# Kernel optimization log

Measured on AMD Instinct MI355X. Metric: run time of the kernel, lower is better.

Reference implementation:

```python
import jax, jax.numpy as jnp
import numpy as np

N = 100000      # nodes
E = 1600000     # edges (avg degree 16)
D_IN = 128
H = 256
OUT = 20
EPS = 1e-5      # BatchNorm1d default eps


def setup_inputs() -> dict:
    key = jax.random.key(0)
    ks = jax.random.split(key, 16)
    s = 0.05  # keep activations bounded across stacked layers
    x = jax.random.normal(ks[0], (N, D_IN), jnp.float32)
    edge_index = jax.random.randint(ks[1], (2, E), 0, N, dtype=jnp.int32)
    W0 = jax.random.normal(ks[2], (D_IN, H), jnp.float32) * s
    W1 = jax.random.normal(ks[3], (H, H), jnp.float32) * s
    W2 = jax.random.normal(ks[4], (H, H), jnp.float32) * s
    W3 = jax.random.normal(ks[5], (H, OUT), jnp.float32) * s
    b0 = jnp.zeros((H,), jnp.float32)
    b1 = jnp.zeros((H,), jnp.float32)
    b2 = jnp.zeros((H,), jnp.float32)
    b3 = jnp.zeros((OUT,), jnp.float32)
    gamma = jnp.ones((3, H), jnp.float32) + 0.1 * jax.random.normal(ks[6], (3, H), jnp.float32)
    beta = 0.1 * jax.random.normal(ks[7], (3, H), jnp.float32)
    run_mean = 0.05 * jax.random.normal(ks[8], (3, H), jnp.float32)
    run_var = jnp.ones((3, H), jnp.float32) + 0.5 * jax.random.uniform(ks[9], (3, H), jnp.float32)
    return {"x": x, "edge_index": edge_index,
            "W0": W0, "b0": b0, "W1": W1, "b1": b1, "W2": W2, "b2": b2,
            "W3": W3, "b3": b3, "gamma": gamma, "beta": beta,
            "run_mean": run_mean, "run_var": run_var}


def _gcn_aggregate(h, src, dst, dinv_sqrt):
    # PyG GCNConv: add self-loops, sym-normalized scatter-add of projected feats.
    coef = (dinv_sqrt[src] * dinv_sqrt[dst])[:, None]          # [E,1]
    agg = jax.ops.segment_sum(h[src] * coef, dst, num_segments=N)
    # self-loop contribution: norm = deg^-1 for i==j
    return agg + h * (dinv_sqrt * dinv_sqrt)[:, None]


def reference(x, edge_index, W0, b0, W1, b1, W2, b2, W3, b3,
              gamma, beta, run_mean, run_var):
    src, dst = edge_index[0], edge_index[1]
    # degree with self-loops (counted on dst, as PyG does on col index)
    deg = jax.ops.segment_sum(jnp.ones((E,), jnp.float32), dst, num_segments=N) + 1.0
    dinv_sqrt = jax.lax.rsqrt(deg)

    h = x
    for i, (W, b) in enumerate([(W0, b0), (W1, b1), (W2, b2)]):
        h = _gcn_aggregate(h @ W, src, dst, dinv_sqrt) + b
        # BatchNorm1d in eval mode (running stats), then ReLU; dropout is identity in eval
        h = (h - run_mean[i]) * jax.lax.rsqrt(run_var[i] + EPS) * gamma[i] + beta[i]
        h = jax.nn.relu(h)
    h = _gcn_aggregate(h @ W3, src, dst, dinv_sqrt) + b3
    return h
```

## Files before the change

kernel.cpp:

```cpp
#include <hip/hip_runtime.h>
#include <hip/hip_bf16.h>
#include <stdint.h>

#define NN 100000
#define NE 1600000
#define BNEPS 1e-5f
#define NBKT 391
#define NBA  256
#define CHUNK ((NE + NBA - 1) / NBA)

using short8 = __attribute__((ext_vector_type(8))) short;
using f32x4  = __attribute__((ext_vector_type(4))) float;

__device__ __forceinline__ float b2f(ushort u) {
  union { uint32_t u; float f; } c; c.u = ((uint32_t)u) << 16; return c.f;
}
__device__ __forceinline__ ushort f2bf(float f) {
  union { float f; uint32_t u; } c; c.f = f;
  uint32_t r = (c.u + 0x7FFFu + ((c.u >> 16) & 1u)) >> 16;
  return (ushort)r;
}
__device__ __forceinline__ uint pk(float a, float b) {
  return (uint)f2bf(a) | ((uint)f2bf(b) << 16);
}
__device__ __forceinline__ void gload16(const void* g, void* lds) {
  __builtin_amdgcn_global_load_lds((const __attribute__((address_space(1))) void*)g,
                                   (__attribute__((address_space(3))) void*)lds,
                                   16, 0, 0);
}
__device__ __forceinline__ void add16(float* a, uint4 q) {
  a[0] += b2f((ushort)(q.x & 0xFFFF)); a[1] += b2f((ushort)(q.x >> 16));
  a[2] += b2f((ushort)(q.y & 0xFFFF)); a[3] += b2f((ushort)(q.y >> 16));
  a[4] += b2f((ushort)(q.z & 0xFFFF)); a[5] += b2f((ushort)(q.z >> 16));
  a[6] += b2f((ushort)(q.w & 0xFFFF)); a[7] += b2f((ushort)(q.w >> 16));
}
__device__ __forceinline__ void set16(float* a, uint4 q) {
  a[0] = b2f((ushort)(q.x & 0xFFFF)); a[1] = b2f((ushort)(q.x >> 16));
  a[2] = b2f((ushort)(q.y & 0xFFFF)); a[3] = b2f((ushort)(q.y >> 16));
  a[4] = b2f((ushort)(q.z & 0xFFFF)); a[5] = b2f((ushort)(q.z >> 16));
  a[6] = b2f((ushort)(q.w & 0xFFFF)); a[7] = b2f((ushort)(q.w >> 16));
}

__global__ __launch_bounds__(256) void k_hist(const int* __restrict__ dst, int* __restrict__ ghist) {
  __shared__ int h[NBKT];
  for (int t = threadIdx.x; t < NBKT; t += 256) h[t] = 0;
  __syncthreads();
  int e0 = blockIdx.x * CHUNK;
  int e1 = e0 + CHUNK; if (e1 > NE) e1 = NE;
  for (int e = e0 + threadIdx.x; e < e1; e += 256)
    atomicAdd(&h[((uint)dst[e]) >> 8], 1);
  __syncthreads();
  for (int t = threadIdx.x; t < NBKT; t += 256) ghist[t * NBA + blockIdx.x] = h[t];
}

__global__ __launch_bounds__(256) void k_gscanA(const int* __restrict__ ghist, int* __restrict__ gbase,
                                                int* __restrict__ btot) {
  __shared__ int s[256];
  int t = threadIdx.x, b = blockIdx.x;
  int d = ghist[b * NBA + t];
  s[t] = d; __syncthreads();
  int val = d;
  for (int sh = 1; sh < 256; sh <<= 1) {
    int tv = (t >= sh) ? s[t - sh] : 0;
    __syncthreads();
    val += tv; s[t] = val;
    __syncthreads();
  }
  gbase[b * NBA + t] = val - d;
  if (t == 255) btot[b] = val;
}

__global__ __launch_bounds__(512) void k_bscan(const int* __restrict__ btot, int* __restrict__ bbase,
                                               int* __restrict__ offs) {
  __shared__ int s[512];
  int t = threadIdx.x;
  int d = (t < NBKT) ? btot[t] : 0;
  s[t] = d; __syncthreads();
  int val = d;
  for (int sh = 1; sh < 512; sh <<= 1) {
    int tv = (t >= sh) ? s[t - sh] : 0;
    __syncthreads();
    val += tv; s[t] = val;
    __syncthreads();
  }
  if (t < NBKT) bbase[t] = val - d;
  if (t == 0) offs[NN] = NE;
}

__global__ __launch_bounds__(256) void k_scatter(const int* __restrict__ src, const int* __restrict__ dst,
                                                 const int* __restrict__ bbase, const int* __restrict__ gbase,
                                                 uint* __restrict__ bpack) {
  __shared__ int lbase[NBKT];
  for (int t = threadIdx.x; t < NBKT; t += 256)
    lbase[t] = bbase[t] + gbase[t * NBA + blockIdx.x];
  __syncthreads();
  int e0 = blockIdx.x * CHUNK;
  int e1 = e0 + CHUNK; if (e1 > NE) e1 = NE;
  for (int e = e0 + threadIdx.x; e < e1; e += 256) {
    int d = dst[e];
    int pos = atomicAdd(&lbase[((uint)d) >> 8], 1);
    bpack[pos] = ((uint)(d & 255) << 17) | (uint)src[e];
  }
}

__global__ __launch_bounds__(256) void k_bucketB(const uint* __restrict__ bpack, const int* __restrict__ btot,
                                                 const int* __restrict__ bbase, int* __restrict__ csrc,
                                                 int* __restrict__ offs, float* __restrict__ dinv) {
  __shared__ int hist[256];
  __shared__ int sc[256];
  __shared__ int loc[256];
  int b = blockIdx.x, t = threadIdx.x;
  int cnt = btot[b], base = bbase[b];
  const uint* bp = bpack + base;
  hist[t] = 0; __syncthreads();
  for (int i = t; i < cnt; i += 256) atomicAdd(&hist[bp[i] >> 17], 1);
  __syncthreads();
  int d = hist[t];
  sc[t] = d; __syncthreads();
  int val = d;
  for (int sh = 1; sh < 256; sh <<= 1) {
    int tv = (t >= sh) ? sc[t - sh] : 0;
    __syncthreads();
    val += tv; sc[t] = val;
    __syncthreads();
  }
  loc[t] = val - d;
  int n = b * 256 + t;
  if (n < NN) {
    offs[n] = base + val - d;
    dinv[n] = rsqrtf((float)d + 1.0f);
  }
  __syncthreads();
  for (int i = t; i < cnt; i += 256) {
    uint p = bp[i];
    int l = p >> 17, s = p & 0x1FFFF;
    int pos = atomicAdd(&loc[l], 1);
    csrc[base + pos] = s;
  }
}

__global__ __launch_bounds__(256) void k_prep(
    const float* __restrict__ W0, const float* __restrict__ W1, const float* __restrict__ W2,
    const float* __restrict__ W3, const float* __restrict__ b0, const float* __restrict__ b1,
    const float* __restrict__ b2, const float* __restrict__ gamma, const float* __restrict__ beta,
    const float* __restrict__ rm, const float* __restrict__ rv,
    ushort* __restrict__ W0t, ushort* __restrict__ W1t, ushort* __restrict__ W2t,
    ushort* __restrict__ W3t, float* __restrict__ bnA, float* __restrict__ bnB) {
  int tid = blockIdx.x * blockDim.x + threadIdx.x;
  int nthr = gridDim.x * blockDim.x;
  for (int i = tid; i < 256 * 128; i += nthr) { int m = i >> 7, k = i & 127; W0t[i] = f2bf(W0[k * 256 + m]); }
  for (int i = tid; i < 256 * 256; i += nthr) {
    int m = i >> 8, k = i & 255;
    W1t[i] = f2bf(W1[k * 256 + m]);
    W2t[i] = f2bf(W2[k * 256 + m]);
  }
  for (int i = tid; i < 32 * 256; i += nthr) {
    int m = i >> 8, k = i & 255;
    W3t[i] = (m < 20) ? f2bf(W3[k * 20 + m]) : (ushort)0;
  }
  for (int i = tid; i < 3 * 256; i += nthr) {
    int l = i >> 8, c = i & 255;
    float A = gamma[i] * rsqrtf(rv[i] + BNEPS);
    float bb = (l == 0) ? b0[c] : (l == 1) ? b1[c] : b2[c];
    bnA[i] = A;
    bnB[i] = (bb - rm[i]) * A + beta[i];
  }
}

__global__ __launch_bounds__(256) void k_convx(const float4* __restrict__ x, uint2* __restrict__ xb,
                                               const float* __restrict__ dinv) {
  int stride = gridDim.x * blockDim.x;
  const int n4 = NN * 128 / 4;
  for (int i = blockIdx.x * blockDim.x + threadIdx.x; i < n4; i += stride) {
    float4 f = x[i];
    float dv = dinv[i >> 5];
    uint2 o;
    o.x = pk(f.x * dv, f.y * dv);
    o.y = pk(f.z * dv, f.w * dv);
    xb[i] = o;
  }
}


__global__ __launch_bounds__(256) void k_agg256(const ushort* __restrict__ Z,
                                                const int* __restrict__ offs, const int* __restrict__ csrc,
                                                const float* __restrict__ dinv, ushort* __restrict__ Outb) {
  int wave = threadIdx.x >> 6, lane = threadIdx.x & 63;
  int v = blockIdx.x * 4 + wave;
  if (v >= NN) return;
  float dv = dinv[v];
  int p = lane >> 5, fl = lane & 31;
  const uint4* Z4 = reinterpret_cast<const uint4*>(Z);
  float acc[8];
  if (p == 0) {
    set16(acc, Z4[(size_t)v * 32 + fl]);
  } else {
#pragma unroll
    for (int j = 0; j < 8; ++j) acc[j] = 0.0f;
  }
  int e1 = offs[v + 1];
  int e = offs[v] + p;
  for (; e + 6 < e1; e += 8) {
    int u0 = csrc[e], u1 = csrc[e + 2], u2 = csrc[e + 4], u3 = csrc[e + 6];
    uint4 q0 = Z4[(size_t)u0 * 32 + fl];
    uint4 q1 = Z4[(size_t)u1 * 32 + fl];
    uint4 q2 = Z4[(size_t)u2 * 32 + fl];
    uint4 q3 = Z4[(size_t)u3 * 32 + fl];
    add16(acc, q0); add16(acc, q1); add16(acc, q2); add16(acc, q3);
  }
  for (; e < e1; e += 2) add16(acc, Z4[(size_t)csrc[e] * 32 + fl]);
#pragma unroll
  for (int j = 0; j < 8; ++j) acc[j] += __shfl_xor(acc[j], 32);
  int o = p * 4;
  uint2 w;
  w.x = pk(acc[o + 0] * dv, acc[o + 1] * dv);
  w.y = pk(acc[o + 2] * dv, acc[o + 3] * dv);
  reinterpret_cast<uint2*>(Outb)[(size_t)v * 64 + fl * 2 + p] = w;
}

__global__ __launch_bounds__(256) void k_agg128(const ushort* __restrict__ Z,
                                                const int* __restrict__ offs, const int* __restrict__ csrc,
                                                const float* __restrict__ dinv, ushort* __restrict__ Outb) {
  int wave = threadIdx.x >> 6, lane = threadIdx.x & 63;
  int v = blockIdx.x * 4 + wave;
  if (v >= NN) return;
  float dv = dinv[v];
  int q = lane >> 4, fl = lane & 15;
  const uint4* Z4 = reinterpret_cast<const uint4*>(Z);
  float acc[8];
  if (q == 0) {
    set16(acc, Z4[(size_t)v * 16 + fl]);
  } else {
#pragma unroll
    for (int j = 0; j < 8; ++j) acc[j] = 0.0f;
  }
  int e1 = offs[v + 1];
  int e = offs[v] + q;
  for (; e + 12 < e1; e += 16) {
    int u0 = csrc[e], u1 = csrc[e + 4], u2 = csrc[e + 8], u3 = csrc[e + 12];
    uint4 q0 = Z4[(size_t)u0 * 16 + fl];
    uint4 q1 = Z4[(size_t)u1 * 16 + fl];
    uint4 q2 = Z4[(size_t)u2 * 16 + fl];
    uint4 q3 = Z4[(size_t)u3 * 16 + fl];
    add16(acc, q0); add16(acc, q1); add16(acc, q2); add16(acc, q3);
  }
  for (; e < e1; e += 4) add16(acc, Z4[(size_t)csrc[e] * 16 + fl]);
#pragma unroll
  for (int j = 0; j < 8; ++j) {
    acc[j] += __shfl_xor(acc[j], 16);
    acc[j] += __shfl_xor(acc[j], 32);
  }
  uint w = pk(acc[2 * q] * dv, acc[2 * q + 1] * dv);
  reinterpret_cast<uint*>(Outb)[(size_t)v * 64 + fl * 4 + q] = w;
}

__global__ __launch_bounds__(256) void k_aggfin(const ushort* __restrict__ Z,
                                                const int* __restrict__ offs, const int* __restrict__ csrc,
                                                const float* __restrict__ dinv, const float* __restrict__ b3,
                                                float* __restrict__ out) {
  int wave = threadIdx.x >> 6, lane = threadIdx.x & 63;
  int v = blockIdx.x * 4 + wave;
  if (v >= NN) return;
  float dv = dinv[v];
  int s = lane >> 3, fl = lane & 7;
  const uint2* Z2 = reinterpret_cast<const uint2*>(Z);
  float acc[4];
  if (s == 0) {
    uint2 qq = Z2[(size_t)v * 8 + fl];
    acc[0] = b2f((ushort)(qq.x & 0xFFFF)); acc[1] = b2f((ushort)(qq.x >> 16));
    acc[2] = b2f((ushort)(qq.y & 0xFFFF)); acc[3] = b2f((ushort)(qq.y >> 16));
  } else {
    acc[0] = acc[1] = acc[2] = acc[3] = 0.0f;
  }
  int e1 = offs[v + 1];
  int e = offs[v] + s;
  for (; e + 8 < e1; e += 16) {
    int u0 = csrc[e], u1 = csrc[e + 8];
    uint2 q0 = Z2[(size_t)u0 * 8 + fl];
    uint2 q1 = Z2[(size_t)u1 * 8 + fl];
    acc[0] += b2f((ushort)(q0.x & 0xFFFF)) + b2f((ushort)(q1.x & 0xFFFF));
    acc[1] += b2f((ushort)(q0.x >> 16))    + b2f((ushort)(q1.x >> 16));
    acc[2] += b2f((ushort)(q0.y & 0xFFFF)) + b2f((ushort)(q1.y & 0xFFFF));
    acc[3] += b2f((ushort)(q0.y >> 16))    + b2f((ushort)(q1.y >> 16));
  }
  for (; e < e1; e += 8) {
    uint2 qq = Z2[(size_t)csrc[e] * 8 + fl];
    acc[0] += b2f((ushort)(qq.x & 0xFFFF)); acc[1] += b2f((ushort)(qq.x >> 16));
    acc[2] += b2f((ushort)(qq.y & 0xFFFF)); acc[3] += b2f((ushort)(qq.y >> 16));
  }
#pragma unroll
  for (int j = 0; j < 4; ++j) {
    acc[j] += __shfl_xor(acc[j], 8);
    acc[j] += __shfl_xor(acc[j], 16);
    acc[j] += __shfl_xor(acc[j], 32);
  }
  if (s == 0 && fl < 5) {
    float4 w;
    w.x = acc[0] * dv + b3[fl * 4 + 0];
    w.y = acc[1] * dv + b3[fl * 4 + 1];
    w.z = acc[2] * dv + b3[fl * 4 + 2];
    w.w = acc[3] * dv + b3[fl * 4 + 3];
    *reinterpret_cast<float4*>(out + (size_t)v * 20 + fl * 4) = w;
  }
}

template<int KT, bool EPI, bool SCALE>
__global__ __launch_bounds__(256) void k_gemm2(const ushort* __restrict__ A,
                                               const ushort* __restrict__ Bt,
                                               ushort* __restrict__ Out,
                                               const float* __restrict__ bnA,
                                               const float* __restrict__ bnB,
                                               const float* __restrict__ dinv) {
  constexpr int BK = 64;
  constexpr int NT = KT / BK;
  __shared__ ushort Ald[2][128 * 64];
  __shared__ ushort Bld[2][128 * 64];
  int tid = threadIdx.x;
  int lane = tid & 63;
  int wave = tid >> 6;
  int wm = wave >> 1, wn = wave & 1;
  size_t row0 = (size_t)blockIdx.y * 128;
  int col0 = blockIdx.x * 128;
  int laneLo = lane & 15, laneHi = lane >> 4;

  f32x4 acc[4][4];
#pragma unroll
  for (int i = 0; i < 4; ++i)
#pragma unroll
    for (int j = 0; j < 4; ++j)
#pragma unroll
      for (int r = 0; r < 4; ++r) acc[i][j][r] = 0.0f;

  auto stage = [&](int buf, int k0) {
#pragma unroll
    for (int is = 0; is < 4; ++is) {
      int idx = is * 256 + tid;
      int r = idx >> 3, c = idx & 7;
      size_t gr = row0 + r; if (gr >= NN) gr = NN - 1;
      gload16(A + gr * KT + k0 + ((c ^ (r & 7)) << 3), &Ald[buf][(idx & ~63) * 8]);
    }
#pragma unroll
    for (int is = 0; is < 4; ++is) {
      int idx = is * 256 + tid;
      int r = idx >> 3, c = idx & 7;
      gload16(Bt + (size_t)(col0 + r) * KT + k0 + ((c ^ (r & 7)) << 3), &Bld[buf][(idx & ~63) * 8]);
    }
  };

  stage(0, 0);
  asm volatile("s_waitcnt vmcnt(0)" ::: "memory");
  __builtin_amdgcn_s_barrier();

  for (int t = 0; t < NT; ++t) {
    int cur = t & 1;
    if (t + 1 < NT) stage(cur ^ 1, (t + 1) * BK);
#pragma unroll
    for (int kk = 0; kk < BK; kk += 32) {
      short8 af[4]; short8 bf[4];
      int slotBase = kk >> 3;
#pragma unroll
      for (int fm = 0; fm < 4; ++fm) {
        int R = wm * 64 + fm * 16 + laneLo;
        int sl = (slotBase + laneHi) ^ (R & 7);
        af[fm] = *reinterpret_cast<const short8*>(&Ald[cur][R * 64 + sl * 8]);
      }
#pragma unroll
      for (int fn = 0; fn < 4; ++fn) {
        int R = wn * 64 + fn * 16 + laneLo;
        int sl = (slotBase + laneHi) ^ (R & 7);
        bf[fn] = *reinterpret_cast<const short8*>(&Bld[cur][R * 64 + sl * 8]);
      }
#pragma unroll
      for (int fm = 0; fm < 4; ++fm)
#pragma unroll
        for (int fn = 0; fn < 4; ++fn)
          acc[fm][fn] = __builtin_amdgcn_mfma_f32_16x16x32_bf16(af[fm], bf[fn], acc[fm][fn], 0, 0, 0);
    }
    asm volatile("s_waitcnt vmcnt(0)" ::: "memory");
    __builtin_amdgcn_s_barrier();
  }

  int lr = laneHi * 4, lc = laneLo;
#pragma unroll
  for (int fm = 0; fm < 4; ++fm) {
#pragma unroll
    for (int r = 0; r < 4; ++r) {
      size_t grow = row0 + wm * 64 + fm * 16 + lr + r;
      if (grow >= NN) continue;
      float ds = 1.0f;
      if constexpr (SCALE) ds = dinv[grow];
#pragma unroll
      for (int fn = 0; fn < 4; ++fn) {
        int gcol = col0 + wn * 64 + fn * 16 + lc;
        float v = acc[fm][fn][r];
        if constexpr (EPI) v = fmaxf(v * bnA[gcol] + bnB[gcol], 0.0f);
        if constexpr (SCALE) v *= ds;
        Out[grow * 256 + gcol] = f2bf(v);
      }
    }
  }
}

template<int KTOT, int BN, bool EPI, bool SCALE>
__global__ __launch_bounds__(256) void k_gemm(const ushort* __restrict__ A,
                                              const ushort* __restrict__ Bt,
                                              ushort* __restrict__ Out,
                                              const float* __restrict__ bnA,
                                              const float* __restrict__ bnB,
                                              const float* __restrict__ dinv, int outW) {
  constexpr int BM = 128, BK = 64;
  constexpr int WN = (BN == 128) ? 64 : 16;
  constexpr int WM = 64;
  constexpr int FM = WM / 16, FN = WN / 16;
  __shared__ ushort Alds[BM * BK];
  __shared__ ushort Blds[BN * BK];
  int tid = threadIdx.x;
  int lane = tid & 63;
  int wave = tid >> 6;
  int wm = wave >> 1, wn = wave & 1;
  size_t row0 = (size_t)blockIdx.x * BM;
  int col0 = blockIdx.y * BN;

  f32x4 acc[FM][FN];
#pragma unroll
  for (int i = 0; i < FM; ++i)
#pragma unroll
    for (int j = 0; j < FN; ++j)
#pragma unroll
      for (int r = 0; r < 4; ++r) acc[i][j][r] = 0.0f;

  for (int k0 = 0; k0 < KTOT; k0 += BK) {
#pragma unroll
    for (int is = 0; is < 4; ++is) {
      int idx = is * 256 + tid;
      int r = idx >> 3, c = idx & 7;
      size_t gr = row0 + r; if (gr >= NN) gr = NN - 1;
      gload16(A + gr * KTOT + k0 + c * 8, &Alds[(size_t)(idx & ~63) * 8]);
    }
#pragma unroll
    for (int is = 0; is < BN / 32; ++is) {
      int idx = is * 256 + tid;
      int r = idx >> 3, c = idx & 7;
      gload16(Bt + (size_t)(col0 + r) * KTOT + k0 + c * 8, &Blds[(size_t)(idx & ~63) * 8]);
    }
    __syncthreads();
#pragma unroll
    for (int kk = 0; kk < BK; kk += 32) {
      short8 af[FM]; short8 bfr[FN];
#pragma unroll
      for (int fm = 0; fm < FM; ++fm)
        af[fm] = *reinterpret_cast<const short8*>(&Alds[(wm * WM + fm * 16 + (lane & 15)) * BK + kk + (lane >> 4) * 8]);
#pragma unroll
      for (int fn = 0; fn < FN; ++fn)
        bfr[fn] = *reinterpret_cast<const short8*>(&Blds[(wn * WN + fn * 16 + (lane & 15)) * BK + kk + (lane >> 4) * 8]);
#pragma unroll
      for (int fm = 0; fm < FM; ++fm)
#pragma unroll
        for (int fn = 0; fn < FN; ++fn)
          acc[fm][fn] = __builtin_amdgcn_mfma_f32_16x16x32_bf16(af[fm], bfr[fn], acc[fm][fn], 0, 0, 0);
    }
    __syncthreads();
  }

  int lr = (lane >> 4) * 4, lc = lane & 15;
#pragma unroll
  for (int fm = 0; fm < FM; ++fm) {
#pragma unroll
    for (int r = 0; r < 4; ++r) {
      size_t grow = row0 + wm * WM + fm * 16 + lr + r;
      if (grow >= NN) continue;
      float ds = 1.0f;
      if constexpr (SCALE) ds = dinv[grow];
#pragma unroll
      for (int fn = 0; fn < FN; ++fn) {
        int gcol = col0 + wn * WN + fn * 16 + lc;
        float v = acc[fm][fn][r];
        if constexpr (EPI) v = fmaxf(v * bnA[gcol] + bnB[gcol], 0.0f);
        if constexpr (SCALE) v *= ds;
        Out[grow * outW + gcol] = f2bf(v);
      }
    }
  }
}

extern "C" void kernel_launch(void* const* d_in, const int* in_sizes, int n_in,
                              void* d_out, int out_size, void* d_ws, size_t ws_size,
                              hipStream_t stream) {
  (void)in_sizes; (void)n_in; (void)out_size; (void)ws_size;
  const float* x     = (const float*)d_in[0];
  const int*   ei    = (const int*)d_in[1];
  const float* W0    = (const float*)d_in[2];
  const float* b0    = (const float*)d_in[3];
  const float* W1    = (const float*)d_in[4];
  const float* b1    = (const float*)d_in[5];
  const float* W2    = (const float*)d_in[6];
  const float* b2    = (const float*)d_in[7];
  const float* W3    = (const float*)d_in[8];
  const float* b3    = (const float*)d_in[9];
  const float* gamma = (const float*)d_in[10];
  const float* beta  = (const float*)d_in[11];
  const float* rm    = (const float*)d_in[12];
  const float* rv    = (const float*)d_in[13];
  const int* src = ei;
  const int* dst = ei + NE;
  float* out = (float*)d_out;

  char* ws = (char*)d_ws;
  size_t off = 0;
  auto alloc = [&](size_t bytes) -> void* {
    void* p = ws + off; off += (bytes + 255) & ~(size_t)255; return p;
  };
  int*    ghist = (int*)alloc((size_t)NBKT * NBA * 4);
  int*    gbase = (int*)alloc((size_t)NBKT * NBA * 4);
  int*    btot  = (int*)alloc(NBKT * 4);
  int*    bbase = (int*)alloc(NBKT * 4);
  uint*   bpack = (uint*)alloc((size_t)NE * 4);
  int*    offs  = (int*)alloc((NN + 1) * (size_t)4);
  int*    csrc  = (int*)alloc((size_t)NE * 4);
  float*  dinv  = (float*)alloc(NN * 4);
  ushort* W0t   = (ushort*)alloc(256 * 128 * 2);
  ushort* W1t   = (ushort*)alloc(256 * 256 * 2);
  ushort* W2t   = (ushort*)alloc(256 * 256 * 2);
  ushort* W3t   = (ushort*)alloc(32 * 256 * 2);
  float*  bnA   = (float*)alloc(3 * 256 * 4);
  float*  bnB   = (float*)alloc(3 * 256 * 4);
  ushort* bufS  = (ushort*)alloc((size_t)NN * 128 * 2);
  ushort* bufA  = (ushort*)alloc((size_t)NN * 256 * 2);
  ushort* bufB  = (ushort*)alloc((size_t)NN * 256 * 2);

  k_hist<<<NBA, 256, 0, stream>>>(dst, ghist);
  k_gscanA<<<NBKT, 256, 0, stream>>>(ghist, gbase, btot);
  k_bscan<<<1, 512, 0, stream>>>(btot, bbase, offs);
  k_scatter<<<NBA, 256, 0, stream>>>(src, dst, bbase, gbase, bpack);
  k_bucketB<<<NBKT, 256, 0, stream>>>(bpack, btot, bbase, csrc, offs, dinv);
  k_prep<<<256, 256, 0, stream>>>(W0, W1, W2, W3, b0, b1, b2, gamma, beta, rm, rv,
                                  W0t, W1t, W2t, W3t, bnA, bnB);
  k_convx<<<2048, 256, 0, stream>>>((const float4*)x, (uint2*)bufS, dinv);

  const int aggBlocks = (NN + 3) / 4;
  dim3 gMain(2, (NN + 127) / 128);
  dim3 gLast((NN + 127) / 128, 1);

  k_agg128<<<aggBlocks, 256, 0, stream>>>(bufS, offs, csrc, dinv, bufA);
  k_gemm2<128, true, true><<<gMain, 256, 0, stream>>>(bufA, W0t, bufB, bnA, bnB, dinv);
  k_agg256<<<aggBlocks, 256, 0, stream>>>(bufB, offs, csrc, dinv, bufA);
  k_gemm2<256, true, true><<<gMain, 256, 0, stream>>>(bufA, W1t, bufB, bnA + 256, bnB + 256, dinv);
  k_agg256<<<aggBlocks, 256, 0, stream>>>(bufB, offs, csrc, dinv, bufA);
  k_gemm2<256, true, false><<<gMain, 256, 0, stream>>>(bufA, W2t, bufB, bnA + 512, bnB + 512, nullptr);
  k_gemm<256, 32, false, true><<<gLast, 256, 0, stream>>>(bufB, W3t, bufS, nullptr, nullptr, dinv, 32);
  k_aggfin<<<aggBlocks, 256, 0, stream>>>(bufS, offs, csrc, dinv, b3, out);
}
```

Before: 538.9 us.

## Widen hidden-layer GEMM to full 256 columns per block and double histogram blocks

The three hidden-layer GEMMs now use 512-thread blocks, each computing a 128x256 output tile. Each A row tile is therefore loaded once instead of once per column half, which halves A traffic. In exchange the LDS double buffering and XOR swizzle are dropped, so loads are no longer overlapped with MFMA compute and LDS reads may hit bank conflicts. The edge-bucketing histogram also doubles its partition count to 512, with the scan resized to match.

```diff
diff --git a/kernel.cpp b/kernel.cpp
--- a/kernel.cpp
+++ b/kernel.cpp
@@ -6,7 +6,7 @@
 #define NE 1600000
 #define BNEPS 1e-5f
 #define NBKT 391
-#define NBA  256
+#define NBA  512
 #define CHUNK ((NE + NBA - 1) / NBA)
 
 using short8 = __attribute__((ext_vector_type(8))) short;
@@ -53,21 +53,21 @@
   for (int t = threadIdx.x; t < NBKT; t += 256) ghist[t * NBA + blockIdx.x] = h[t];
 }
 
-__global__ __launch_bounds__(256) void k_gscanA(const int* __restrict__ ghist, int* __restrict__ gbase,
+__global__ __launch_bounds__(512) void k_gscanA(const int* __restrict__ ghist, int* __restrict__ gbase,
                                                 int* __restrict__ btot) {
-  __shared__ int s[256];
+  __shared__ int s[NBA];
   int t = threadIdx.x, b = blockIdx.x;
   int d = ghist[b * NBA + t];
   s[t] = d; __syncthreads();
   int val = d;
-  for (int sh = 1; sh < 256; sh <<= 1) {
+  for (int sh = 1; sh < NBA; sh <<= 1) {
     int tv = (t >= sh) ? s[t - sh] : 0;
     __syncthreads();
     val += tv; s[t] = val;
     __syncthreads();
   }
   gbase[b * NBA + t] = val - d;
-  if (t == 255) btot[b] = val;
+  if (t == NBA - 1) btot[b] = val;
 }
 
 __global__ __launch_bounds__(512) void k_bscan(const int* __restrict__ btot, int* __restrict__ bbase,
@@ -305,7 +305,7 @@
 }
 
 template<int KT, bool EPI, bool SCALE>
-__global__ __launch_bounds__(256) void k_gemm2(const ushort* __restrict__ A,
+__global__ __launch_bounds__(512) void k_gemmW(const ushort* __restrict__ A,
                                                const ushort* __restrict__ Bt,
                                                ushort* __restrict__ Out,
                                                const float* __restrict__ bnA,
@@ -313,14 +313,13 @@
                                                const float* __restrict__ dinv) {
   constexpr int BK = 64;
   constexpr int NT = KT / BK;
-  __shared__ ushort Ald[2][128 * 64];
-  __shared__ ushort Bld[2][128 * 64];
+  __shared__ ushort Alds[128 * 64];
+  __shared__ ushort Blds[256 * 64];
   int tid = threadIdx.x;
   int lane = tid & 63;
   int wave = tid >> 6;
-  int wm = wave >> 1, wn = wave & 1;
-  size_t row0 = (size_t)blockIdx.y * 128;
-  int col0 = blockIdx.x * 128;
+  int wm = wave >> 2, wn = wave & 3;
+  size_t row0 = (size_t)blockIdx.x * 128;
   int laneLo = lane & 15, laneHi = lane >> 4;
 
   f32x4 acc[4][4];
@@ -331,53 +330,38 @@
 #pragma unroll
       for (int r = 0; r < 4; ++r) acc[i][j][r] = 0.0f;
 
-  auto stage = [&](int buf, int k0) {
-#pragma unroll
-    for (int is = 0; is < 4; ++is) {
-      int idx = is * 256 + tid;
+  for (int t = 0; t < NT; ++t) {
+    int k0 = t * BK;
+#pragma unroll
+    for (int is = 0; is < 2; ++is) {
+      int idx = is * 512 + tid;
       int r = idx >> 3, c = idx & 7;
       size_t gr = row0 + r; if (gr >= NN) gr = NN - 1;
-      gload16(A + gr * KT + k0 + ((c ^ (r & 7)) << 3), &Ald[buf][(idx & ~63) * 8]);
+      gload16(A + gr * KT + k0 + c * 8, &Alds[(idx & ~63) * 8]);
     }
 #pragma unroll
     for (int is = 0; is < 4; ++is) {
-      int idx = is * 256 + tid;
+      int idx = is * 512 + tid;
       int r = idx >> 3, c = idx & 7;
-      gload16(Bt + (size_t)(col0 + r) * KT + k0 + ((c ^ (r & 7)) << 3), &Bld[buf][(idx & ~63) * 8]);
-    }
-  };
-
-  stage(0, 0);
-  asm volatile("s_waitcnt vmcnt(0)" ::: "memory");
-  __builtin_amdgcn_s_barrier();
-
-  for (int t = 0; t < NT; ++t) {
-    int cur = t & 1;
-    if (t + 1 < NT) stage(cur ^ 1, (t + 1) * BK);
+      gload16(Bt + (size_t)r * KT + k0 + c * 8, &Blds[(idx & ~63) * 8]);
+    }
+    __syncthreads();
 #pragma unroll
     for (int kk = 0; kk < BK; kk += 32) {
       short8 af[4]; short8 bf[4];
-      int slotBase = kk >> 3;
-#pragma unroll
-      for (int fm = 0; fm < 4; ++fm) {
-        int R = wm * 64 + fm * 16 + laneLo;
-        int sl = (slotBase + laneHi) ^ (R & 7);
-        af[fm] = *reinterpret_cast<const short8*>(&Ald[cur][R * 64 + sl * 8]);
-      }
-#pragma unroll
-      for (int fn = 0; fn < 4; ++fn) {
-        int R = wn * 64 + fn * 16 + laneLo;
-        int sl = (slotBase + laneHi) ^ (R & 7);
-        bf[fn] = *reinterpret_cast<const short8*>(&Bld[cur][R * 64 + sl * 8]);
-      }
+#pragma unroll
+      for (int fm = 0; fm < 4; ++fm)
+        af[fm] = *reinterpret_cast<const short8*>(&Alds[(wm * 64 + fm * 16 + laneLo) * 64 + kk + laneHi * 8]);
+#pragma unroll
+      for (int fn = 0; fn < 4; ++fn)
+        bf[fn] = *reinterpret_cast<const short8*>(&Blds[(wn * 64 + fn * 16 + laneLo) * 64 + kk + laneHi * 8]);
 #pragma unroll
       for (int fm = 0; fm < 4; ++fm)
 #pragma unroll
         for (int fn = 0; fn < 4; ++fn)
           acc[fm][fn] = __builtin_amdgcn_mfma_f32_16x16x32_bf16(af[fm], bf[fn], acc[fm][fn], 0, 0, 0);
     }
-    asm volatile("s_waitcnt vmcnt(0)" ::: "memory");
-    __builtin_amdgcn_s_barrier();
+    __syncthreads();
   }
 
   int lr = laneHi * 4, lc = laneLo;
@@ -391,7 +375,7 @@
       if constexpr (SCALE) ds = dinv[grow];
 #pragma unroll
       for (int fn = 0; fn < 4; ++fn) {
-        int gcol = col0 + wn * 64 + fn * 16 + lc;
+        int gcol = wn * 64 + fn * 16 + lc;
         float v = acc[fm][fn][r];
         if constexpr (EPI) v = fmaxf(v * bnA[gcol] + bnB[gcol], 0.0f);
         if constexpr (SCALE) v *= ds;
@@ -529,7 +513,7 @@
   ushort* bufB  = (ushort*)alloc((size_t)NN * 256 * 2);
 
   k_hist<<<NBA, 256, 0, stream>>>(dst, ghist);
-  k_gscanA<<<NBKT, 256, 0, stream>>>(ghist, gbase, btot);
+  k_gscanA<<<NBKT, NBA, 0, stream>>>(ghist, gbase, btot);
   k_bscan<<<1, 512, 0, stream>>>(btot, bbase, offs);
   k_scatter<<<NBA, 256, 0, stream>>>(src, dst, bbase, gbase, bpack);
   k_bucketB<<<NBKT, 256, 0, stream>>>(bpack, btot, bbase, csrc, offs, dinv);
@@ -538,15 +522,15 @@
   k_convx<<<2048, 256, 0, stream>>>((const float4*)x, (uint2*)bufS, dinv);
 
   const int aggBlocks = (NN + 3) / 4;
-  dim3 gMain(2, (NN + 127) / 128);
-  dim3 gLast((NN + 127) / 128, 1);
+  const int gemmBlocks = (NN + 127) / 128;
+  dim3 gLast(gemmBlocks, 1);
 
   k_agg128<<<aggBlocks, 256, 0, stream>>>(bufS, offs, csrc, dinv, bufA);
-  k_gemm2<128, true, true><<<gMain, 256, 0, stream>>>(bufA, W0t, bufB, bnA, bnB, dinv);
+  k_gemmW<128, true, true><<<gemmBlocks, 512, 0, stream>>>(bufA, W0t, bufB, bnA, bnB, dinv);
   k_agg256<<<aggBlocks, 256, 0, stream>>>(bufB, offs, csrc, dinv, bufA);
-  k_gemm2<256, true, true><<<gMain, 256, 0, stream>>>(bufA, W1t, bufB, bnA + 256, bnB + 256, dinv);
+  k_gemmW<256, true, true><<<gemmBlocks, 512, 0, stream>>>(bufA, W1t, bufB, bnA + 256, bnB + 256, dinv);
   k_agg256<<<aggBlocks, 256, 0, stream>>>(bufB, offs, csrc, dinv, bufA);
-  k_gemm2<256, true, false><<<gMain, 256, 0, stream>>>(bufA, W2t, bufB, bnA + 512, bnB + 512, nullptr);
+  k_gemmW<256, true, false><<<gemmBlocks, 512, 0, stream>>>(bufA, W2t, bufB, bnA + 512, bnB + 512, nullptr);
   k_gemm<256, 32, false, true><<<gLast, 256, 0, stream>>>(bufB, W3t, bufS, nullptr, nullptr, dinv, 32);
   k_aggfin<<<aggBlocks, 256, 0, stream>>>(bufS, offs, csrc, dinv, b3, out);
 }
```

Result: slower. 551.6 us (+2.4%).
